# Performance work log

Hardware: AMD Instinct MI355X
Metric: run time of the kernel (lower is better)

The kernel has to match this reference:

```python
import jax, jax.numpy as jnp
import numpy as np

D_MODEL = 1024
E_MODEL = 2
D_STATE = 16
D_CONV = 4
D_IN = E_MODEL * D_MODEL            # 2048
DT_RANK = int(np.ceil(D_MODEL / 16))  # 64
B_SZ, SEQ = 1, 2048


def setup_inputs() -> dict:
    key = jax.random.key(0)
    ks = jax.random.split(key, 9)
    s = lambda fan: 1.0 / np.sqrt(fan)
    return {
        "x": jax.random.normal(ks[0], (B_SZ, SEQ, D_MODEL), jnp.float32),
        "W_in": jax.random.normal(ks[1], (D_MODEL, 2 * D_IN), jnp.float32) * s(D_MODEL),
        "conv_w": jax.random.normal(ks[2], (D_CONV, D_IN), jnp.float32) * s(D_CONV),
        "conv_b": jnp.zeros((D_IN,), jnp.float32),
        "W_x": jax.random.normal(ks[3], (D_IN, DT_RANK + 2 * D_STATE), jnp.float32) * s(D_IN),
        "W_dt": jax.random.normal(ks[4], (DT_RANK, D_IN), jnp.float32) * s(DT_RANK),
        "b_dt": jax.random.normal(ks[5], (D_IN,), jnp.float32) * 0.01,
        "D": jnp.ones((D_IN,), jnp.float32),
        "W_out": jax.random.normal(ks[6], (D_IN, D_MODEL), jnp.float32) * s(D_IN),
    }


def _causal_depthwise_conv(x, w, b):
    # x: (b, l, d_in); w: (d_conv, d_in) depthwise taps; causal left pad
    L = x.shape[1]
    xp = jnp.pad(x, ((0, 0), (D_CONV - 1, 0), (0, 0)))
    y = b
    for k in range(D_CONV):  # small fixed kernel width
        y = y + xp[:, k:k + L, :] * w[k]
    return y


def _selective_scan(u, delta, A, Bm, Cm, D):
    # u, delta: (b,l,d); A: (d,n); Bm, Cm: (b,l,n); D: (d,)
    dA = jnp.einsum('bld,dn->bldn', delta, A)
    dB_u = jnp.einsum('bld,bld,bln->bldn', delta, u, Bm)
    # replicate tf.pad(dA[:,1:], [[0,0],[1,1],[0,0],[0,0]])[:,1:]
    t = jnp.pad(dA[:, 1:], ((0, 0), (1, 1), (0, 0), (0, 0)))[:, 1:]
    t = jnp.flip(t, axis=1)
    t = jnp.cumsum(t, axis=1)
    dA_cs = jnp.flip(jnp.exp(t), axis=1)
    xs = jnp.cumsum(dB_u * dA_cs, axis=1) / (dA_cs + 1e-12)
    y = jnp.einsum('bldn,bln->bld', xs, Cm)
    return y + u * D


def reference(x, W_in, conv_w, conv_b, W_x, W_dt, b_dt, D, W_out):
    seq_len = x.shape[1]
    x_and_res = x @ W_in                                  # (b,l,2*d_in)
    xi, res = jnp.split(x_and_res, [D_IN], axis=-1)
    xi = _causal_depthwise_conv(xi, conv_w, conv_b)[:, :seq_len, :]
    xi = jax.nn.swish(xi)
    # SSM
    A = -jnp.exp(jnp.log(jnp.arange(1, D_STATE + 1, dtype=jnp.float32)))  # (n,)
    A = jnp.broadcast_to(A, (D_IN, D_STATE))
    x_dbl = xi @ W_x                                      # (b,l,dtr+2n)
    delta, Bm, Cm = jnp.split(x_dbl, [DT_RANK, DT_RANK + D_STATE], axis=-1)
    delta = jax.nn.softplus(delta @ W_dt + b_dt)          # (b,l,d_in)
    y = _selective_scan(xi, delta, A, Bm, Cm, D)
    y = y * jax.nn.swish(res)
    return y @ W_out
```

## Files before the change

kernel.cpp:

```cpp
#include <hip/hip_runtime.h>
#include <hip/hip_bf16.h>

#define L_SEQ 2048
#define DMODEL 1024
#define DIN 2048
#define DTR 64
#define NST 16
#define CCH 128
#define CHL 16

typedef unsigned short u16;
typedef __bf16 bf16x8 __attribute__((ext_vector_type(8)));
typedef float f32x4 __attribute__((ext_vector_type(4)));

__device__ inline u16 f2bf(float v) {
    __bf16 h = (__bf16)v;
    return __builtin_bit_cast(unsigned short, h);
}
__device__ inline float bf2f(u16 v) {
    __bf16 h = __builtin_bit_cast(__bf16, v);
    return (float)h;
}
__device__ inline float rcpf(float x) { return __builtin_amdgcn_rcpf(x); }
__device__ inline float swishf(float v) { return v * rcpf(1.f + __expf(-v)); }
__device__ inline float softplusf(float v) {
    return (v > 20.f) ? v : __logf(1.f + __expf(v));
}

__device__ inline void powers16(float v, float* p) {
    p[0] = v;
    p[1] = v * v;
    p[2] = p[1] * v;
    p[3] = p[1] * p[1];
    p[4] = p[3] * p[0];  p[5] = p[3] * p[1];  p[6] = p[3] * p[2];  p[7] = p[3] * p[3];
    p[8] = p[7] * p[0];  p[9] = p[7] * p[1];  p[10] = p[7] * p[2]; p[11] = p[7] * p[3];
    p[12] = p[7] * p[4]; p[13] = p[7] * p[5]; p[14] = p[7] * p[6]; p[15] = p[7] * p[7];
}

template<int TBN, int EPI>
__global__ __launch_bounds__(256) void gemm_bf16(const u16* __restrict__ A,
                                                 const u16* __restrict__ Bt,
                                                 float* __restrict__ C,
                                                 const float* __restrict__ bias,
                                                 u16* __restrict__ xiraw,
                                                 float* __restrict__ gate,
                                                 int M, int N, int K) {
    constexpr int LDSZ = (128 + TBN) * 64;
    constexpr int ROUNDS = (128 + TBN) / 32;
    constexpr int FN = TBN / 32;
    __shared__ u16 smem[2 * LDSZ];

    const int tid = threadIdx.x;
    const int lane = tid & 63;
    const int wid = tid >> 6;
    const int wm = wid >> 1;
    const int wn = wid & 1;
    const int bm = blockIdx.y * 128;
    const int bn = blockIdx.x * TBN;

    const int srow8 = lane >> 3;
    const int schunk = lane & 7;
    const int sgchunk = schunk ^ srow8;
    const int lm = lane & 15;
    const int lk = lane >> 4;

    f32x4 acc[4][FN];
#pragma unroll
    for (int i = 0; i < 4; ++i)
#pragma unroll
        for (int j = 0; j < FN; ++j) acc[i][j] = (f32x4){0.f, 0.f, 0.f, 0.f};

    auto stage = [&](int buf, int t) {
        const int k0 = t * 64;
        u16* base = smem + buf * LDSZ;
#pragma unroll
        for (int rr = 0; rr < ROUNDS; ++rr) {
            int row = rr * 32 + wid * 8;
            int grow = row + srow8;
            const u16* src;
            if (row < 128) src = A + (size_t)(bm + grow) * K + k0 + sgchunk * 8;
            else           src = Bt + (size_t)(bn + grow - 128) * K + k0 + sgchunk * 8;
            u16* dst = base + row * 64;
            __builtin_amdgcn_global_load_lds(
                (const __attribute__((address_space(1))) void*)src,
                (__attribute__((address_space(3))) void*)dst, 16, 0, 0);
        }
    };

    auto compute = [&](int buf) {
        const u16* base = smem + buf * LDSZ;
#pragma unroll
        for (int kk = 0; kk < 2; ++kk) {
            bf16x8 av[4], bv[FN];
#pragma unroll
            for (int fm = 0; fm < 4; ++fm) {
                int row = wm * 64 + fm * 16 + lm;
                int slot = (kk * 4 + lk) ^ (row & 7);
                av[fm] = *(const bf16x8*)(base + row * 64 + slot * 8);
            }
#pragma unroll
            for (int fn = 0; fn < FN; ++fn) {
                int row = 128 + wn * (TBN / 2) + fn * 16 + lm;
                int slot = (kk * 4 + lk) ^ (row & 7);
                bv[fn] = *(const bf16x8*)(base + row * 64 + slot * 8);
            }
#pragma unroll
            for (int fm = 0; fm < 4; ++fm)
#pragma unroll
                for (int fn = 0; fn < FN; ++fn)
                    acc[fm][fn] = __builtin_amdgcn_mfma_f32_16x16x32_bf16(av[fm], bv[fn], acc[fm][fn], 0, 0, 0);
        }
    };

    const int nt = K / 64;
    int cur = 0;
    stage(0, 0);
    for (int t = 0; t < nt - 1; ++t) {
        stage(cur ^ 1, t + 1);
        asm volatile("s_waitcnt vmcnt(%0) lgkmcnt(0)\n\ts_barrier"
                     :: "n"(ROUNDS) : "memory");
        compute(cur);
        asm volatile("s_waitcnt lgkmcnt(0)\n\ts_barrier" ::: "memory");
        cur ^= 1;
    }
    asm volatile("s_waitcnt vmcnt(0) lgkmcnt(0)\n\ts_barrier" ::: "memory");
    compute(cur);

#pragma unroll
    for (int fm = 0; fm < 4; ++fm) {
#pragma unroll
        for (int fn = 0; fn < FN; ++fn) {
            int col = bn + wn * (TBN / 2) + fn * 16 + lm;
            if (EPI == 1) {
                float b = bias[col];
                float4 o;
                o.x = softplusf(acc[fm][fn][0] + b);
                o.y = softplusf(acc[fm][fn][1] + b);
                o.z = softplusf(acc[fm][fn][2] + b);
                o.w = softplusf(acc[fm][fn][3] + b);
                int rowb = bm + wm * 64 + fm * 16 + lk * 4;
                *(float4*)(C + (size_t)col * M + rowb) = o;
            } else {
#pragma unroll
                for (int j = 0; j < 4; ++j) {
                    int row = bm + wm * 64 + fm * 16 + lk * 4 + j;
                    float v = acc[fm][fn][j];
                    if (EPI == 0) {
                        C[(size_t)row * N + col] = v;
                    } else {
                        if (col < DIN) xiraw[(size_t)row * DIN + col] = f2bf(v);
                        else           gate[(size_t)row * DIN + (col - DIN)] = swishf(v);
                    }
                }
            }
        }
    }
}

__global__ __launch_bounds__(256) void gemm_bf16_sk(const u16* __restrict__ A, int lda,
                                                    const u16* __restrict__ Bt, int ldb,
                                                    float* __restrict__ P,
                                                    int M, int N, int K, int kc) {
    constexpr int TBN = 32;
    constexpr int LDSZ = (128 + TBN) * 64;
    constexpr int ROUNDS = (128 + TBN) / 32;
    __shared__ u16 smem[2 * LDSZ];

    const int tid = threadIdx.x;
    const int lane = tid & 63;
    const int wid = tid >> 6;
    const int wm = wid >> 1;
    const int wn = wid & 1;
    const int bm = blockIdx.y * 128;
    const int bn = blockIdx.x * TBN;
    const int kbeg = blockIdx.z * kc;
    float* Cz = P + (size_t)blockIdx.z * M * N;

    const int srow8 = lane >> 3;
    const int schunk = lane & 7;
    const int sgchunk = schunk ^ srow8;
    const int lm = lane & 15;
    const int lk = lane >> 4;

    f32x4 acc[4];
#pragma unroll
    for (int i = 0; i < 4; ++i) acc[i] = (f32x4){0.f, 0.f, 0.f, 0.f};

    auto stage = [&](int buf, int t) {
        const int k0 = kbeg + t * 64;
        u16* base = smem + buf * LDSZ;
#pragma unroll
        for (int rr = 0; rr < ROUNDS; ++rr) {
            int row = rr * 32 + wid * 8;
            int grow = row + srow8;
            const u16* src;
            if (row < 128) src = A + (size_t)(bm + grow) * lda + k0 + sgchunk * 8;
            else           src = Bt + (size_t)(bn + grow - 128) * ldb + k0 + sgchunk * 8;
            u16* dst = base + row * 64;
            __builtin_amdgcn_global_load_lds(
                (const __attribute__((address_space(1))) void*)src,
                (__attribute__((address_space(3))) void*)dst, 16, 0, 0);
        }
    };

    auto compute = [&](int buf) {
        const u16* base = smem + buf * LDSZ;
#pragma unroll
        for (int kk = 0; kk < 2; ++kk) {
            bf16x8 av[4], bv;
#pragma unroll
            for (int fm = 0; fm < 4; ++fm) {
                int row = wm * 64 + fm * 16 + lm;
                int slot = (kk * 4 + lk) ^ (row & 7);
                av[fm] = *(const bf16x8*)(base + row * 64 + slot * 8);
            }
            {
                int row = 128 + wn * 16 + lm;
                int slot = (kk * 4 + lk) ^ (row & 7);
                bv = *(const bf16x8*)(base + row * 64 + slot * 8);
            }
#pragma unroll
            for (int fm = 0; fm < 4; ++fm)
                acc[fm] = __builtin_amdgcn_mfma_f32_16x16x32_bf16(av[fm], bv, acc[fm], 0, 0, 0);
        }
    };

    const int nt = kc / 64;
    int cur = 0;
    stage(0, 0);
    for (int t = 0; t < nt - 1; ++t) {
        stage(cur ^ 1, t + 1);
        asm volatile("s_waitcnt vmcnt(%0) lgkmcnt(0)\n\ts_barrier"
                     :: "n"(ROUNDS) : "memory");
        compute(cur);
        asm volatile("s_waitcnt lgkmcnt(0)\n\ts_barrier" ::: "memory");
        cur ^= 1;
    }
    asm volatile("s_waitcnt vmcnt(0) lgkmcnt(0)\n\ts_barrier" ::: "memory");
    compute(cur);

#pragma unroll
    for (int fm = 0; fm < 4; ++fm) {
        int col = bn + wn * 16 + lm;
#pragma unroll
        for (int j = 0; j < 4; ++j) {
            int row = bm + wm * 64 + fm * 16 + lk * 4 + j;
            Cz[(size_t)row * N + col] = acc[fm][j];
        }
    }
}

__device__ inline void castT_dev(const float* __restrict__ W, u16* __restrict__ Wt,
                                 int K, int N, int bx, int by) {
    __shared__ u16 tile[64][65];
    int n0 = bx * 64, k0 = by * 64;
    int tn = threadIdx.x & 63, t4 = threadIdx.x >> 6;
#pragma unroll
    for (int j = 0; j < 16; ++j) {
        int k = t4 + j * 4;
        if (n0 + tn < N) tile[tn][k] = f2bf(W[(size_t)(k0 + k) * N + n0 + tn]);
    }
    __syncthreads();
#pragma unroll
    for (int j = 0; j < 16; ++j) {
        int n = t4 + j * 4;
        if (n0 + n < N) Wt[(size_t)(n0 + n) * K + k0 + tn] = tile[n][tn];
    }
}

__global__ __launch_bounds__(256) void prep_fused(const float* __restrict__ x,
                                                  const float* __restrict__ W_in,
                                                  const float* __restrict__ W_x,
                                                  const float* __restrict__ W_dt,
                                                  const float* __restrict__ W_out,
                                                  u16* __restrict__ xbf,
                                                  u16* __restrict__ WinT,
                                                  u16* __restrict__ WxT,
                                                  u16* __restrict__ WdtT,
                                                  u16* __restrict__ WoutT) {
    int b = blockIdx.x;
    if (b < 2048) {
        int i = b * 256 + threadIdx.x;
        float4 v = ((const float4*)x)[i];
        ushort4 o;
        o.x = f2bf(v.x); o.y = f2bf(v.y); o.z = f2bf(v.z); o.w = f2bf(v.w);
        ((ushort4*)xbf)[i] = o;
    } else if (b < 3072) {
        int t = b - 2048;
        castT_dev(W_in, WinT, DMODEL, 4096, t & 63, t >> 6);
    } else if (b < 3136) {
        int t = b - 3072;
        castT_dev(W_x, WxT, DIN, 96, t & 1, t >> 1);
    } else if (b < 3168) {
        int t = b - 3136;
        castT_dev(W_dt, WdtT, DTR, DIN, t, 0);
    } else {
        int t = b - 3168;
        castT_dev(W_out, WoutT, DIN, DMODEL, t & 15, t >> 4);
    }
}

__global__ __launch_bounds__(256) void reduce_sk(const float* __restrict__ P,
                                                 float* __restrict__ xdbl,
                                                 u16* __restrict__ xdbf) {
    int i = blockIdx.x * 256 + threadIdx.x;
    float s = 0.f;
#pragma unroll
    for (int z = 0; z < 4; ++z) s += P[z * (L_SEQ * 96) + i];
    xdbl[i] = s;
    int l = i / 96, k = i - l * 96;
    if (k < DTR) xdbf[l * DTR + k] = f2bf(s);
}

__global__ __launch_bounds__(256) void conv_swish(const u16* __restrict__ xiraw,
                                                  const float* __restrict__ cw,
                                                  const float* __restrict__ cb,
                                                  u16* __restrict__ xib) {
    int id = blockIdx.x * 256 + threadIdx.x;
    int l = id >> 11;
    int d = id & (DIN - 1);
    float acc = cb[d];
#pragma unroll
    for (int k = 0; k < 4; ++k) {
        int ls = l - 3 + k;
        if (ls >= 0) acc += bf2f(xiraw[ls * DIN + d]) * cw[k * DIN + d];
    }
    xib[id] = f2bf(swishf(acc));
}

__global__ __launch_bounds__(256) void scanA(const float* __restrict__ deltaT,
                                             const u16* __restrict__ u,
                                             const float* __restrict__ xdbl,
                                             float* __restrict__ localQ,
                                             float* __restrict__ csum) {
    __shared__ float sh[CHL][16];
    const int tid = threadIdx.x;
    const int c = blockIdx.y;
    const int d = blockIdx.x * 256 + tid;
    const int l0 = c * CHL;
    {
        int l = tid >> 4, j = tid & 15;
        sh[l][j] = xdbl[(l0 + l) * 96 + DTR + j];
    }
    __syncthreads();
    float dl[CHL];
    {
        const float4* dp = (const float4*)(deltaT + (size_t)d * L_SEQ + l0);
        float4 v0 = dp[0], v1 = dp[1], v2 = dp[2], v3 = dp[3];
        dl[0] = v0.x; dl[1] = v0.y; dl[2] = v0.z; dl[3] = v0.w;
        dl[4] = v1.x; dl[5] = v1.y; dl[6] = v1.z; dl[7] = v1.w;
        dl[8] = v2.x; dl[9] = v2.y; dl[10] = v2.z; dl[11] = v2.w;
        dl[12] = v3.x; dl[13] = v3.y; dl[14] = v3.z; dl[15] = v3.w;
    }
    u16 uls[CHL];
#pragma unroll
    for (int l = 0; l < CHL; ++l) uls[l] = u[(l0 + l) * DIN + d];

    float q[16];
#pragma unroll
    for (int n = 0; n < 16; ++n) q[n] = 0.f;
    float s = 0.f;
#pragma unroll 4
    for (int l = 0; l < CHL; ++l) {
        float dlv = dl[l];
        float ulv = bf2f(uls[l]);
        float bb[16];
        const float4* shv = (const float4*)&sh[l][0];
        *(float4*)&bb[0] = shv[0];  *(float4*)&bb[4] = shv[1];
        *(float4*)&bb[8] = shv[2];  *(float4*)&bb[12] = shv[3];
        float v = __expf(-dlv);
        float p[16];
        powers16(v, p);
        float dlul = dlv * ulv;
#pragma unroll
        for (int n = 0; n < 16; ++n) q[n] = q[n] * p[n] + dlul * bb[n];
        s += dlv;
    }
    float* dst = localQ + (size_t)(c * DIN + d) * 16;
    *(float4*)(dst + 0)  = make_float4(q[0], q[1], q[2], q[3]);
    *(float4*)(dst + 4)  = make_float4(q[4], q[5], q[6], q[7]);
    *(float4*)(dst + 8)  = make_float4(q[8], q[9], q[10], q[11]);
    *(float4*)(dst + 12) = make_float4(q[12], q[13], q[14], q[15]);
    csum[c * DIN + d] = s;
}

__global__ __launch_bounds__(256) void scanB(float* __restrict__ localQ,
                                             const float* __restrict__ csum,
                                             float* __restrict__ send) {
    int gid = blockIdx.x * 256 + threadIdx.x;
    int n = gid & 15;
    int d = gid >> 4;
    const float An = -(float)(n + 1);
    float q = 0.f;
#pragma unroll 4
    for (int c = 0; c < CCH; ++c) {
        float cs = csum[c * DIN + d];
        float w = __expf(An * cs);
        float* lq = localQ + (size_t)(c * DIN + d) * 16 + n;
        float lv = *lq;
        *lq = q;
        q = q * w + lv;
    }
    if (n == 0) {
        double ssum = 0.0;
        for (int c = CCH - 1; c >= 0; --c) {
            ssum += (double)csum[c * DIN + d];
            send[c * DIN + d] = (float)ssum;
        }
    }
}

__global__ __launch_bounds__(256) void scanC(const float* __restrict__ deltaT,
                                             const u16* __restrict__ u,
                                             const float* __restrict__ xdbl,
                                             const float* __restrict__ localQ,
                                             const float* __restrict__ send,
                                             const float* __restrict__ Dvec,
                                             const float* __restrict__ gate,
                                             u16* __restrict__ ybf) {
    __shared__ float sh[CHL][32];
    const int tid = threadIdx.x;
    const int c = blockIdx.y;
    const int d = blockIdx.x * 256 + tid;
    const int l0 = c * CHL;
#pragma unroll
    for (int k = 0; k < 2; ++k) {
        int idx = tid + k * 256;
        int l = idx >> 5, j = idx & 31;
        sh[l][j] = xdbl[(l0 + l) * 96 + DTR + j];
    }
    __syncthreads();
    float dl[CHL];
    {
        const float4* dp = (const float4*)(deltaT + (size_t)d * L_SEQ + l0);
        float4 v0 = dp[0], v1 = dp[1], v2 = dp[2], v3 = dp[3];
        dl[0] = v0.x; dl[1] = v0.y; dl[2] = v0.z; dl[3] = v0.w;
        dl[4] = v1.x; dl[5] = v1.y; dl[6] = v1.z; dl[7] = v1.w;
        dl[8] = v2.x; dl[9] = v2.y; dl[10] = v2.z; dl[11] = v2.w;
        dl[12] = v3.x; dl[13] = v3.y; dl[14] = v3.z; dl[15] = v3.w;
    }
    u16 uls[CHL];
#pragma unroll
    for (int l = 0; l < CHL; ++l) uls[l] = u[(l0 + l) * DIN + d];

    float q[16];
    {
        const float* src = localQ + (size_t)(c * DIN + d) * 16;
        float4 t0 = *(const float4*)(src + 0);
        float4 t1 = *(const float4*)(src + 4);
        float4 t2 = *(const float4*)(src + 8);
        float4 t3 = *(const float4*)(src + 12);
        q[0] = t0.x; q[1] = t0.y; q[2] = t0.z; q[3] = t0.w;
        q[4] = t1.x; q[5] = t1.y; q[6] = t1.z; q[7] = t1.w;
        q[8] = t2.x; q[9] = t2.y; q[10] = t2.z; q[11] = t2.w;
        q[12] = t3.x; q[13] = t3.y; q[14] = t3.z; q[15] = t3.w;
    }
    const float send_cd = send[c * DIN + d];
    const float Dd = Dvec[d];
    float s = 0.f;
#pragma unroll 4
    for (int l = 0; l < CHL; ++l) {
        float dlv = dl[l];
        float ulv = bf2f(uls[l]);
        float bb[32];
        const float4* shv = (const float4*)&sh[l][0];
        *(float4*)&bb[0]  = shv[0]; *(float4*)&bb[4]  = shv[1];
        *(float4*)&bb[8]  = shv[2]; *(float4*)&bb[12] = shv[3];
        *(float4*)&bb[16] = shv[4]; *(float4*)&bb[20] = shv[5];
        *(float4*)&bb[24] = shv[6]; *(float4*)&bb[28] = shv[7];
        float v = __expf(-dlv);
        float p[16];
        powers16(v, p);
        float dlul = dlv * ulv;
#pragma unroll
        for (int n = 0; n < 16; ++n) q[n] = q[n] * p[n] + dlul * bb[n];
        s += dlv;
        float suf = send_cd - s;
        float contrib;
        float ac[4] = {0.f, 0.f, 0.f, 0.f};
        if (suf < 0.8f) {
#pragma unroll
            for (int n = 0; n < 16; ++n) ac[n & 3] += q[n] * bb[16 + n];
            contrib = (ac[0] + ac[1]) + (ac[2] + ac[3]);
        } else {
            float w = __expf(-suf);
            float e[16];
            powers16(w, e);
            if (suf > 40.f) {
#pragma unroll
                for (int n = 0; n < 16; ++n) ac[n & 3] += (q[n] * e[n]) * bb[16 + n];
                contrib = ((ac[0] + ac[1]) + (ac[2] + ac[3])) * 1e12f;
            } else {
#pragma unroll
                for (int n = 0; n < 16; ++n) {
                    float g = e[n] * rcpf(e[n] + 1e-12f);
                    ac[n & 3] += (q[n] * g) * bb[16 + n];
                }
                contrib = (ac[0] + ac[1]) + (ac[2] + ac[3]);
            }
        }
        float y = contrib + ulv * Dd;
        ybf[(l0 + l) * DIN + d] = f2bf(y * gate[(l0 + l) * DIN + d]);
    }
}

extern "C" void kernel_launch(void* const* d_in, const int* in_sizes, int n_in,
                              void* d_out, int out_size, void* d_ws, size_t ws_size,
                              hipStream_t stream) {
    const float* x      = (const float*)d_in[0];
    const float* W_in   = (const float*)d_in[1];
    const float* conv_w = (const float*)d_in[2];
    const float* conv_b = (const float*)d_in[3];
    const float* W_x    = (const float*)d_in[4];
    const float* W_dt   = (const float*)d_in[5];
    const float* b_dt   = (const float*)d_in[6];
    const float* Dvec   = (const float*)d_in[7];
    const float* W_out  = (const float*)d_in[8];
    float* out = (float*)d_out;

    float* ws = (float*)d_ws;
    u16*   xiraw  = (u16*)ws;
    float* gate   = ws + 2097152;
    u16*   xibf   = (u16*)(ws + 6291456);
    float* xdbl   = ws + 8388608;
    float* deltaT = ws + 8585216;
    float* localQ = ws + 12779520;
    float* csum   = ws + 16973824;
    float* send   = ws + 17235968;
    u16*   xbf    = (u16*)(ws + 17498112);
    u16*   WinT   = (u16*)(ws + 18546688);
    u16*   WxT    = (u16*)(ws + 20643840);
    u16*   WdtT   = (u16*)(ws + 20742144);
    u16*   WoutT  = (u16*)(ws + 20807680);
    u16*   xdbf   = (u16*)(ws + 21856256);
    float* Psk    = ws + 21921792;
    u16*   ybf    = (u16*)(ws + 22708224);

    prep_fused<<<3680, 256, 0, stream>>>(x, W_in, W_x, W_dt, W_out,
                                         xbf, WinT, WxT, WdtT, WoutT);
    gemm_bf16<64, 2><<<dim3(4096 / 64, L_SEQ / 128), 256, 0, stream>>>(
        xbf, WinT, nullptr, nullptr, xiraw, gate, L_SEQ, 4096, DMODEL);
    conv_swish<<<(L_SEQ * DIN) / 256, 256, 0, stream>>>(xiraw, conv_w, conv_b, xibf);
    gemm_bf16_sk<<<dim3(3, L_SEQ / 128, 4), 256, 0, stream>>>(
        xibf, DIN, WxT, DIN, Psk, L_SEQ, 96, DIN, 512);
    reduce_sk<<<(L_SEQ * 96) / 256, 256, 0, stream>>>(Psk, xdbl, xdbf);
    gemm_bf16<64, 1><<<dim3(DIN / 64, L_SEQ / 128), 256, 0, stream>>>(
        xdbf, WdtT, deltaT, b_dt, nullptr, nullptr, L_SEQ, DIN, DTR);
    scanA<<<dim3(DIN / 256, CCH), 256, 0, stream>>>(deltaT, xibf, xdbl, localQ, csum);
    scanB<<<(DIN * NST) / 256, 256, 0, stream>>>(localQ, csum, send);
    scanC<<<dim3(DIN / 256, CCH), 256, 0, stream>>>(deltaT, xibf, xdbl, localQ, send,
                                                    Dvec, gate, ybf);
    gemm_bf16<32, 0><<<dim3(DMODEL / 32, L_SEQ / 128), 256, 0, stream>>>(
        ybf, WoutT, out, nullptr, nullptr, nullptr, L_SEQ, DMODEL, DIN);
}
```

Measured before the change: 154.7 us.

## Fuse split-K reduction into delta GEMM and scans, store gate as bf16

Removes the reduce_sk kernel. The 4-way split-K partial sums are now added directly inside a new single-tile gemm_delta kernel, which also applies bias and softplus, and inside the scanA/scanC prologues that read B/C. The swish gate is stored as bf16 instead of fp32, which halves its write and read traffic. This saves one launch and an intermediate round trip, but the same partial sums are summed several times and the gate loses precision.

```diff
diff --git a/kernel.cpp b/kernel.cpp
--- a/kernel.cpp
+++ b/kernel.cpp
@@ -8,6 +8,7 @@
 #define NST 16
 #define CCH 128
 #define CHL 16
+#define PSKST (L_SEQ * 96)
 
 typedef unsigned short u16;
 typedef __bf16 bf16x8 __attribute__((ext_vector_type(8)));
@@ -41,9 +42,8 @@
 __global__ __launch_bounds__(256) void gemm_bf16(const u16* __restrict__ A,
                                                  const u16* __restrict__ Bt,
                                                  float* __restrict__ C,
-                                                 const float* __restrict__ bias,
                                                  u16* __restrict__ xiraw,
-                                                 float* __restrict__ gate,
+                                                 u16* __restrict__ gateb,
                                                  int M, int N, int K) {
     constexpr int LDSZ = (128 + TBN) * 64;
     constexpr int ROUNDS = (128 + TBN) / 32;
@@ -131,26 +131,15 @@
 #pragma unroll
         for (int fn = 0; fn < FN; ++fn) {
             int col = bn + wn * (TBN / 2) + fn * 16 + lm;
-            if (EPI == 1) {
-                float b = bias[col];
-                float4 o;
-                o.x = softplusf(acc[fm][fn][0] + b);
-                o.y = softplusf(acc[fm][fn][1] + b);
-                o.z = softplusf(acc[fm][fn][2] + b);
-                o.w = softplusf(acc[fm][fn][3] + b);
-                int rowb = bm + wm * 64 + fm * 16 + lk * 4;
-                *(float4*)(C + (size_t)col * M + rowb) = o;
-            } else {
-#pragma unroll
-                for (int j = 0; j < 4; ++j) {
-                    int row = bm + wm * 64 + fm * 16 + lk * 4 + j;
-                    float v = acc[fm][fn][j];
-                    if (EPI == 0) {
-                        C[(size_t)row * N + col] = v;
-                    } else {
-                        if (col < DIN) xiraw[(size_t)row * DIN + col] = f2bf(v);
-                        else           gate[(size_t)row * DIN + (col - DIN)] = swishf(v);
-                    }
+#pragma unroll
+            for (int j = 0; j < 4; ++j) {
+                int row = bm + wm * 64 + fm * 16 + lk * 4 + j;
+                float v = acc[fm][fn][j];
+                if (EPI == 0) {
+                    C[(size_t)row * N + col] = v;
+                } else {
+                    if (col < DIN) xiraw[(size_t)row * DIN + col] = f2bf(v);
+                    else           gateb[(size_t)row * DIN + (col - DIN)] = f2bf(swishf(v));
                 }
             }
         }
@@ -246,6 +235,89 @@
         for (int j = 0; j < 4; ++j) {
             int row = bm + wm * 64 + fm * 16 + lk * 4 + j;
             Cz[(size_t)row * N + col] = acc[fm][j];
+        }
+    }
+}
+
+__global__ __launch_bounds__(256) void gemm_delta(const float* __restrict__ Psk,
+                                                  const u16* __restrict__ WdtT,
+                                                  float* __restrict__ deltaT,
+                                                  const float* __restrict__ bias) {
+    constexpr int TBN = 64;
+    __shared__ u16 smem[(128 + TBN) * 64];
+    const int tid = threadIdx.x;
+    const int lane = tid & 63;
+    const int wid = tid >> 6;
+    const int wm = wid >> 1;
+    const int wn = wid & 1;
+    const int bm = blockIdx.y * 128;
+    const int bn = blockIdx.x * TBN;
+    const int srow8 = lane >> 3;
+    const int schunk = lane & 7;
+    const int sgchunk = schunk ^ srow8;
+    const int lm = lane & 15;
+    const int lk = lane >> 4;
+
+#pragma unroll
+    for (int rr = 0; rr < 2; ++rr) {
+        int row = rr * 32 + wid * 8;
+        int grow = row + srow8;
+        const u16* src = WdtT + (size_t)(bn + grow) * 64 + sgchunk * 8;
+        u16* dst = smem + (128 + row) * 64;
+        __builtin_amdgcn_global_load_lds(
+            (const __attribute__((address_space(1))) void*)src,
+            (__attribute__((address_space(3))) void*)dst, 16, 0, 0);
+    }
+#pragma unroll
+    for (int i = 0; i < 32; ++i) {
+        int idx = tid + i * 256;
+        int r = idx >> 6;
+        int k = idx & 63;
+        size_t off = (size_t)(bm + r) * 96 + k;
+        float s = Psk[off] + Psk[off + PSKST] + Psk[off + 2 * PSKST] + Psk[off + 3 * PSKST];
+        smem[r * 64 + (((k >> 3) ^ (r & 7)) << 3) + (k & 7)] = f2bf(s);
+    }
+    asm volatile("s_waitcnt vmcnt(0) lgkmcnt(0)\n\ts_barrier" ::: "memory");
+
+    f32x4 acc[4][2];
+#pragma unroll
+    for (int i = 0; i < 4; ++i)
+#pragma unroll
+        for (int j = 0; j < 2; ++j) acc[i][j] = (f32x4){0.f, 0.f, 0.f, 0.f};
+#pragma unroll
+    for (int kk = 0; kk < 2; ++kk) {
+        bf16x8 av[4], bv[2];
+#pragma unroll
+        for (int fm = 0; fm < 4; ++fm) {
+            int row = wm * 64 + fm * 16 + lm;
+            int slot = (kk * 4 + lk) ^ (row & 7);
+            av[fm] = *(const bf16x8*)(smem + row * 64 + slot * 8);
+        }
+#pragma unroll
+        for (int fn = 0; fn < 2; ++fn) {
+            int row = 128 + wn * 32 + fn * 16 + lm;
+            int slot = (kk * 4 + lk) ^ (row & 7);
+            bv[fn] = *(const bf16x8*)(smem + row * 64 + slot * 8);
+        }
+#pragma unroll
+        for (int fm = 0; fm < 4; ++fm)
+#pragma unroll
+            for (int fn = 0; fn < 2; ++fn)
+                acc[fm][fn] = __builtin_amdgcn_mfma_f32_16x16x32_bf16(av[fm], bv[fn], acc[fm][fn], 0, 0, 0);
+    }
+#pragma unroll
+    for (int fm = 0; fm < 4; ++fm) {
+#pragma unroll
+        for (int fn = 0; fn < 2; ++fn) {
+            int col = bn + wn * 32 + fn * 16 + lm;
+            float b = bias[col];
+            float4 o;
+            o.x = softplusf(acc[fm][fn][0] + b);
+            o.y = softplusf(acc[fm][fn][1] + b);
+            o.z = softplusf(acc[fm][fn][2] + b);
+            o.w = softplusf(acc[fm][fn][3] + b);
+            int rowb = bm + wm * 64 + fm * 16 + lk * 4;
+            *(float4*)(deltaT + (size_t)col * L_SEQ + rowb) = o;
         }
     }
 }
@@ -300,18 +372,6 @@
     }
 }
 
-__global__ __launch_bounds__(256) void reduce_sk(const float* __restrict__ P,
-                                                 float* __restrict__ xdbl,
-                                                 u16* __restrict__ xdbf) {
-    int i = blockIdx.x * 256 + threadIdx.x;
-    float s = 0.f;
-#pragma unroll
-    for (int z = 0; z < 4; ++z) s += P[z * (L_SEQ * 96) + i];
-    xdbl[i] = s;
-    int l = i / 96, k = i - l * 96;
-    if (k < DTR) xdbf[l * DTR + k] = f2bf(s);
-}
-
 __global__ __launch_bounds__(256) void conv_swish(const u16* __restrict__ xiraw,
                                                   const float* __restrict__ cw,
                                                   const float* __restrict__ cb,
@@ -330,7 +390,7 @@
 
 __global__ __launch_bounds__(256) void scanA(const float* __restrict__ deltaT,
                                              const u16* __restrict__ u,
-                                             const float* __restrict__ xdbl,
+                                             const float* __restrict__ Psk,
                                              float* __restrict__ localQ,
                                              float* __restrict__ csum) {
     __shared__ float sh[CHL][16];
@@ -340,7 +400,8 @@
     const int l0 = c * CHL;
     {
         int l = tid >> 4, j = tid & 15;
-        sh[l][j] = xdbl[(l0 + l) * 96 + DTR + j];
+        size_t off = (size_t)(l0 + l) * 96 + DTR + j;
+        sh[l][j] = Psk[off] + Psk[off + PSKST] + Psk[off + 2 * PSKST] + Psk[off + 3 * PSKST];
     }
     __syncthreads();
     float dl[CHL];
@@ -412,11 +473,11 @@
 
 __global__ __launch_bounds__(256) void scanC(const float* __restrict__ deltaT,
                                              const u16* __restrict__ u,
-                                             const float* __restrict__ xdbl,
+                                             const float* __restrict__ Psk,
                                              const float* __restrict__ localQ,
                                              const float* __restrict__ send,
                                              const float* __restrict__ Dvec,
-                                             const float* __restrict__ gate,
+                                             const u16* __restrict__ gateb,
                                              u16* __restrict__ ybf) {
     __shared__ float sh[CHL][32];
     const int tid = threadIdx.x;
@@ -427,7 +488,8 @@
     for (int k = 0; k < 2; ++k) {
         int idx = tid + k * 256;
         int l = idx >> 5, j = idx & 31;
-        sh[l][j] = xdbl[(l0 + l) * 96 + DTR + j];
+        size_t off = (size_t)(l0 + l) * 96 + DTR + j;
+        sh[l][j] = Psk[off] + Psk[off + PSKST] + Psk[off + 2 * PSKST] + Psk[off + 3 * PSKST];
     }
     __syncthreads();
     float dl[CHL];
@@ -500,7 +562,8 @@
             }
         }
         float y = contrib + ulv * Dd;
-        ybf[(l0 + l) * DIN + d] = f2bf(y * gate[(l0 + l) * DIN + d]);
+        float gv = bf2f(gateb[(l0 + l) * DIN + d]);
+        ybf[(l0 + l) * DIN + d] = f2bf(y * gv);
     }
 }
 
@@ -520,36 +583,33 @@
 
     float* ws = (float*)d_ws;
     u16*   xiraw  = (u16*)ws;
-    float* gate   = ws + 2097152;
-    u16*   xibf   = (u16*)(ws + 6291456);
-    float* xdbl   = ws + 8388608;
-    float* deltaT = ws + 8585216;
-    float* localQ = ws + 12779520;
-    float* csum   = ws + 16973824;
-    float* send   = ws + 17235968;
-    u16*   xbf    = (u16*)(ws + 17498112);
-    u16*   WinT   = (u16*)(ws + 18546688);
-    u16*   WxT    = (u16*)(ws + 20643840);
-    u16*   WdtT   = (u16*)(ws + 20742144);
-    u16*   WoutT  = (u16*)(ws + 20807680);
-    u16*   xdbf   = (u16*)(ws + 21856256);
-    float* Psk    = ws + 21921792;
-    u16*   ybf    = (u16*)(ws + 22708224);
+    u16*   gateb  = (u16*)(ws + 2097152);
+    u16*   xibf   = (u16*)(ws + 4194304);
+    float* deltaT = ws + 6291456;
+    float* localQ = ws + 10485760;
+    float* csum   = ws + 14680064;
+    float* send   = ws + 14942208;
+    u16*   xbf    = (u16*)(ws + 15204352);
+    u16*   WinT   = (u16*)(ws + 16252928);
+    u16*   WxT    = (u16*)(ws + 18350080);
+    u16*   WdtT   = (u16*)(ws + 18448384);
+    u16*   WoutT  = (u16*)(ws + 18513920);
+    float* Psk    = ws + 19562496;
+    u16*   ybf    = (u16*)(ws + 20348928);
 
     prep_fused<<<3680, 256, 0, stream>>>(x, W_in, W_x, W_dt, W_out,
                                          xbf, WinT, WxT, WdtT, WoutT);
     gemm_bf16<64, 2><<<dim3(4096 / 64, L_SEQ / 128), 256, 0, stream>>>(
-        xbf, WinT, nullptr, nullptr, xiraw, gate, L_SEQ, 4096, DMODEL);
+        xbf, WinT, nullptr, xiraw, gateb, L_SEQ, 4096, DMODEL);
     conv_swish<<<(L_SEQ * DIN) / 256, 256, 0, stream>>>(xiraw, conv_w, conv_b, xibf);
     gemm_bf16_sk<<<dim3(3, L_SEQ / 128, 4), 256, 0, stream>>>(
         xibf, DIN, WxT, DIN, Psk, L_SEQ, 96, DIN, 512);
-    reduce_sk<<<(L_SEQ * 96) / 256, 256, 0, stream>>>(Psk, xdbl, xdbf);
-    gemm_bf16<64, 1><<<dim3(DIN / 64, L_SEQ / 128), 256, 0, stream>>>(
-        xdbf, WdtT, deltaT, b_dt, nullptr, nullptr, L_SEQ, DIN, DTR);
-    scanA<<<dim3(DIN / 256, CCH), 256, 0, stream>>>(deltaT, xibf, xdbl, localQ, csum);
+    gemm_delta<<<dim3(DIN / 64, L_SEQ / 128), 256, 0, stream>>>(
+        Psk, WdtT, deltaT, b_dt);
+    scanA<<<dim3(DIN / 256, CCH), 256, 0, stream>>>(deltaT, xibf, Psk, localQ, csum);
     scanB<<<(DIN * NST) / 256, 256, 0, stream>>>(localQ, csum, send);
-    scanC<<<dim3(DIN / 256, CCH), 256, 0, stream>>>(deltaT, xibf, xdbl, localQ, send,
-                                                    Dvec, gate, ybf);
+    scanC<<<dim3(DIN / 256, CCH), 256, 0, stream>>>(deltaT, xibf, Psk, localQ, send,
+                                                    Dvec, gateb, ybf);
     gemm_bf16<32, 0><<<dim3(DMODEL / 32, L_SEQ / 128), 256, 0, stream>>>(
-        ybf, WoutT, out, nullptr, nullptr, nullptr, L_SEQ, DMODEL, DIN);
-}
+        ybf, WoutT, out, nullptr, nullptr, L_SEQ, DMODEL, DIN);
+}
```

After: 156.8 us. No clear change (+1.3%).
